# Kernel optimization log

Measured on AMD Instinct MI355X. Metric: run time of the kernel, lower is better.

Reference implementation:

```python
import jax, jax.numpy as jnp
import numpy as np

B, CIN, NF, COUT, H, W = 128, 64, 16, 256, 20, 20


def _warp(features, f):
    # features: (B, Cin, r, c), f: (r, c, 2) flow offsets
    r, c = features.shape[2], features.shape[3]
    grid = jnp.stack(
        jnp.meshgrid(jnp.arange(r, dtype=f.dtype), jnp.arange(c, dtype=f.dtype), indexing='ij'),
        axis=-1,
    )  # (r, c, 2) base index map
    idx = grid + f  # index_map += inverse, inverse == flow[i] after double negation
    base = jnp.floor(idx)
    frac = jax.lax.stop_gradient(idx - base)  # torch detaches s and t
    s, t = frac[..., 0], frac[..., 1]
    b = base.astype(jnp.int32)
    bx, by = b[..., 0], b[..., 1]
    padded = jnp.pad(features, ((0, 0), (0, 0), (1, 1), (1, 1)))  # zero pad by 1

    def gather(ix, iy):
        cx = jnp.clip(ix, 0, r)
        cy = jnp.clip(iy, 0, c)
        return padded[:, :, cx + 1, cy + 1]  # (B, Cin, r, c)

    # NOTE: weight for base_10 is s*(1-t) in the original source (apparent bug,
    # should be (1-s)*t) -- replicated here for faithfulness.
    w00 = (1 - s) * (1 - t)
    w01 = s * (1 - t)
    w10 = s * (1 - t)
    w11 = s * t
    return (gather(bx, by) * w00 + gather(bx + 1, by) * w01
            + gather(bx, by + 1) * w10 + gather(bx + 1, by + 1) * w11)


def setup_inputs() -> dict:
    key = jax.random.key(0)
    k1, k2, k3, k4 = jax.random.split(key, 4)
    x = jax.random.normal(k1, (B, CIN, H, W), dtype=jnp.float32)
    flow = jax.random.normal(k2, (NF, H, W, 2), dtype=jnp.float32)
    combinator = jax.random.normal(k3, (COUT, CIN * NF), dtype=jnp.float32) / np.sqrt(CIN * NF)
    bias = jax.random.normal(k4, (COUT,), dtype=jnp.float32) / np.sqrt(CIN * NF)
    return {"x": x, "flow": flow, "combinator": combinator, "bias": bias}


def reference(x, flow, combinator, bias):
    # per-flow bilinear warp, vectorized over the flow axis
    warped = jax.vmap(lambda f: _warp(x, f))(flow)  # (nf, B, Cin, h, w)
    nf, b, cin, h, w = warped.shape
    # permute(1,3,4,2,0).reshape -> columns ordered channel-major, flow-minor
    feat = warped.transpose(1, 3, 4, 2, 0).reshape(b, h, w, cin * nf)
    out = jnp.einsum('bhwk,ok->bhwo', feat, combinator) + bias
    return out.transpose(0, 3, 1, 2)  # (B, Cout, h, w)
```

## Files before the change

kernel.cpp:

```cpp
#include <hip/hip_runtime.h>
#include <hip/hip_fp16.h>
#include <stdint.h>

#define BATCH 128
#define CIN   64
#define NFLOW 16
#define COUT  256
#define HH    20
#define WW    20
#define NPIX  400
#define KTOT  1024
#define PT    100
#define NPT   4
#define NTH   512
#define NFR   7
#define FLR   112

typedef __attribute__((ext_vector_type(8))) short sh8;
typedef __attribute__((ext_vector_type(4))) float f4;

__global__ void prep_w(const float* __restrict__ wg, __half* __restrict__ Wf) {
    int gid = blockIdx.x * 256 + threadIdx.x;
    int j8  = gid & 127;
    int row = gid >> 7;
    int kc16 = j8 >> 2;
    int h    = j8 & 3;
    __half* dst = Wf + ((size_t)(kc16 * 16 + (row >> 4)) * 64 + h * 16 + (row & 15)) * 8;
    #pragma unroll
    for (int j = 0; j < 8; ++j) {
        int kp = j8 * 8 + j;
        int kc = kp >> 6;
        int l  = kp & 63;
        int f  = (kc >> 3) * 8 + (l >> 3);
        int c  = (kc & 7) * 8 + (l & 7);
        dst[j] = __float2half(wg[(size_t)row * KTOT + c * NFLOW + f]);
    }
}

__global__ __launch_bounds__(NTH, 4) void flow_main(
    const float* __restrict__ xg, const __half* __restrict__ Wf,
    const float* __restrict__ flowg, const float* __restrict__ biasg,
    float* __restrict__ outg)
{
    __shared__ __align__(16) __half xb[CIN * NPIX];
    __shared__ __align__(16) __half fl[2][FLR * 64];

    const int bid0 = blockIdx.x;
    const int bid  = (bid0 & 7) * 64 + (bid0 >> 3);
    const int b  = bid >> 2;
    const int pt = bid & 3;
    const int p0 = pt * PT;

    const int tid  = threadIdx.x;
    const int wv   = tid >> 6;
    const int lane = tid & 63;
    const int lr   = lane & 15;
    const int hq   = lane >> 4;

    const float* xsrc = xg + (size_t)b * (CIN * NPIX);

    #pragma unroll
    for (int it = 0; it < 7; ++it) {
        int idx = it * NTH + tid;
        if (idx < 3200) {
            int cb  = idx / NPIX;
            int pix = idx - cb * NPIX;
            const float* s = xsrc + (size_t)(cb * 8) * NPIX + pix;
            __half2 h0 = __floats2half2_rn(s[0 * NPIX], s[1 * NPIX]);
            __half2 h1 = __floats2half2_rn(s[2 * NPIX], s[3 * NPIX]);
            __half2 h2 = __floats2half2_rn(s[4 * NPIX], s[5 * NPIX]);
            __half2 h3 = __floats2half2_rn(s[6 * NPIX], s[7 * NPIX]);
            uint4 pk;
            pk.x = __builtin_bit_cast(uint32_t, h0);
            pk.y = __builtin_bit_cast(uint32_t, h1);
            pk.z = __builtin_bit_cast(uint32_t, h2);
            pk.w = __builtin_bit_cast(uint32_t, h3);
            *(uint4*)&xb[(size_t)idx * 8] = pk;
        }
    }

    __half2 w2_[2][4];
    int     pb_[2][4];
    int     fo_[2];

    auto build_tables = [&](int fb) {
        #pragma unroll
        for (int it = 0; it < 2; ++it) {
            if (it == 0 || lane < PT - 64) {
                int p  = it * 64 + lane;
                int f  = fb * 8 + wv;
                int gp = p0 + p;
                int i = gp / WW;
                int j = gp - i * WW;
                float fx = flowg[((f * HH + i) * WW + j) * 2 + 0];
                float fy = flowg[((f * HH + i) * WW + j) * 2 + 1];
                float ax = (float)i + fx;
                float ay = (float)j + fy;
                float bxf = floorf(ax), byf = floorf(ay);
                float s = ax - bxf, t = ay - byf;
                int ibx = (int)bxf, iby = (int)byf;
                float w00 = (1.f - s) * (1.f - t);
                float w01 = s * (1.f - t);
                float w10 = s * (1.f - t);
                float w11 = s * t;
                int cx0 = min(max(ibx, 0), HH);
                int cx1 = min(max(ibx + 1, 0), HH);
                int cy0 = min(max(iby, 0), WW);
                int cy1 = min(max(iby + 1, 0), WW);
                int v0 = (cx0 < HH) & (cy0 < WW);
                int v1 = (cx1 < HH) & (cy0 < WW);
                int v2 = (cx0 < HH) & (cy1 < WW);
                int v3 = (cx1 < HH) & (cy1 < WW);
                w2_[it][0] = __half2half2(__float2half(v0 ? w00 : 0.f));
                w2_[it][1] = __half2half2(__float2half(v1 ? w01 : 0.f));
                w2_[it][2] = __half2half2(__float2half(v2 ? w10 : 0.f));
                w2_[it][3] = __half2half2(__float2half(v3 ? w11 : 0.f));
                pb_[it][0] = (v0 ? (cx0 * WW + cy0) : 0) * 16;
                pb_[it][1] = (v1 ? (cx1 * WW + cy0) : 0) * 16;
                pb_[it][2] = (v2 ? (cx0 * WW + cy1) : 0) * 16;
                pb_[it][3] = (v3 ? (cx1 * WW + cy1) : 0) * 16;
                fo_[it] = p * 128 + ((wv ^ (p & 7)) << 4);
            }
        }
    };

    auto fill = [&](int k) {
        const char* xcb = (const char*)xb + (k & 7) * 6400;
        char* flb = (char*)fl[k & 1];
        #pragma unroll
        for (int it = 0; it < 2; ++it) {
            if (it == 0 || lane < PT - 64) {
                __half2 s0 = __builtin_bit_cast(__half2, 0u);
                __half2 s1 = s0, s2 = s0, s3 = s0;
                #pragma unroll
                for (int q = 0; q < 4; ++q) {
                    const uint4 d = *(const uint4*)(xcb + pb_[it][q]);
                    __half2 wq = w2_[it][q];
                    s0 = __hfma2(wq, __builtin_bit_cast(__half2, d.x), s0);
                    s1 = __hfma2(wq, __builtin_bit_cast(__half2, d.y), s1);
                    s2 = __hfma2(wq, __builtin_bit_cast(__half2, d.z), s2);
                    s3 = __hfma2(wq, __builtin_bit_cast(__half2, d.w), s3);
                }
                uint4 pk;
                pk.x = __builtin_bit_cast(uint32_t, s0);
                pk.y = __builtin_bit_cast(uint32_t, s1);
                pk.z = __builtin_bit_cast(uint32_t, s2);
                pk.w = __builtin_bit_cast(uint32_t, s3);
                *(uint4*)(flb + fo_[it]) = pk;
            }
        }
    };

    build_tables(0);
    __syncthreads();
    fill(0);
    __syncthreads();

    f4 acc[2][NFR] = {};

    const int q0 = (hq ^ (lr & 7)) << 4;

    for (int kc = 0; kc < 16; ++kc) {
        if (kc == 7) build_tables(1);

        const sh8* wfp = (const sh8*)Wf + (size_t)(2 * kc * 16 + 2 * wv) * 64 + lane;
        sh8 a00 = wfp[0];
        sh8 a01 = wfp[64];
        sh8 a10 = wfp[1024];
        sh8 a11 = wfp[1088];

        if (kc <= 14) fill(kc + 1);

        const char* flr_b = (const char*)fl[kc & 1];
        __builtin_amdgcn_s_setprio(1);
        #pragma unroll
        for (int nf = 0; nf < NFR; ++nf) {
            int rowb = (nf * 16 + lr) * 128;
            sh8 b0 = *(const sh8*)(flr_b + (rowb + q0));
            acc[0][nf] = __builtin_amdgcn_mfma_f32_16x16x32_f16(a00, b0, acc[0][nf], 0, 0, 0);
            acc[1][nf] = __builtin_amdgcn_mfma_f32_16x16x32_f16(a01, b0, acc[1][nf], 0, 0, 0);
            sh8 b1 = *(const sh8*)(flr_b + ((rowb + q0) ^ 64));
            acc[0][nf] = __builtin_amdgcn_mfma_f32_16x16x32_f16(a10, b1, acc[0][nf], 0, 0, 0);
            acc[1][nf] = __builtin_amdgcn_mfma_f32_16x16x32_f16(a11, b1, acc[1][nf], 0, 0, 0);
        }
        __builtin_amdgcn_s_setprio(0);

        __syncthreads();
    }

    float* ob = outg + (size_t)b * (COUT * NPIX) + p0;
    #pragma unroll
    for (int mi = 0; mi < 2; ++mi) {
        #pragma unroll
        for (int r = 0; r < 4; ++r) {
            int m = (wv * 2 + mi) * 16 + hq * 4 + r;
            float bs = biasg[m];
            #pragma unroll
            for (int nf = 0; nf < NFR; ++nf) {
                if (nf < 6 || lr < 4)
                    ob[(size_t)m * NPIX + nf * 16 + lr] = acc[mi][nf][r] + bs;
            }
        }
    }
}

extern "C" void kernel_launch(void* const* d_in, const int* in_sizes, int n_in,
                              void* d_out, int out_size, void* d_ws, size_t ws_size,
                              hipStream_t stream) {
    const float* x    = (const float*)d_in[0];
    const float* flow = (const float*)d_in[1];
    const float* comb = (const float*)d_in[2];
    const float* bias = (const float*)d_in[3];
    float* out = (float*)d_out;

    __half* Wf = (__half*)d_ws;

    prep_w<<<dim3(128), dim3(256), 0, stream>>>(comb, Wf);
    flow_main<<<dim3(BATCH * NPT), dim3(NTH), 0, stream>>>(x, Wf, flow, bias, out);
}
```

Before: 49.25 us.

## Halve block to 4 waves, each computing 64 output channels

The block shrinks from 8 waves to 4. Each wave now owns 64 output rows (four 16-row M tiles) instead of 32, and builds warp tables for two flows instead of one. Each B fragment loaded from shared memory is reused across four MFMAs instead of two, cutting LDS reads per MFMA and giving more independent MFMA chains. The cost is higher register pressure (twice the accumulators and tables), lower occupancy bound, and twice the per-wave warp-fill and x-staging work.

```diff
diff --git a/kernel.cpp b/kernel.cpp
--- a/kernel.cpp
+++ b/kernel.cpp
@@ -12,7 +12,7 @@
 #define KTOT  1024
 #define PT    100
 #define NPT   4
-#define NTH   512
+#define NTH   256
 #define NFR   7
 #define FLR   112
 
@@ -37,7 +37,7 @@
     }
 }
 
-__global__ __launch_bounds__(NTH, 4) void flow_main(
+__global__ __launch_bounds__(NTH, 2) void flow_main(
     const float* __restrict__ xg, const __half* __restrict__ Wf,
     const float* __restrict__ flowg, const float* __restrict__ biasg,
     float* __restrict__ outg)
@@ -60,7 +60,7 @@
     const float* xsrc = xg + (size_t)b * (CIN * NPIX);
 
     #pragma unroll
-    for (int it = 0; it < 7; ++it) {
+    for (int it = 0; it < 13; ++it) {
         int idx = it * NTH + tid;
         if (idx < 3200) {
             int cb  = idx / NPIX;
@@ -79,16 +79,18 @@
         }
     }
 
-    __half2 w2_[2][4];
-    int     pb_[2][4];
-    int     fo_[2];
+    __half2 w2_[4][4];
+    int     pb_[4][4];
+    int     fo_[4];
 
     auto build_tables = [&](int fb) {
         #pragma unroll
-        for (int it = 0; it < 2; ++it) {
+        for (int g = 0; g < 4; ++g) {
+            int it = g & 1;
             if (it == 0 || lane < PT - 64) {
+                int fi = wv * 2 + (g >> 1);
                 int p  = it * 64 + lane;
-                int f  = fb * 8 + wv;
+                int f  = fb * 8 + fi;
                 int gp = p0 + p;
                 int i = gp / WW;
                 int j = gp - i * WW;
@@ -111,15 +113,15 @@
                 int v1 = (cx1 < HH) & (cy0 < WW);
                 int v2 = (cx0 < HH) & (cy1 < WW);
                 int v3 = (cx1 < HH) & (cy1 < WW);
-                w2_[it][0] = __half2half2(__float2half(v0 ? w00 : 0.f));
-                w2_[it][1] = __half2half2(__float2half(v1 ? w01 : 0.f));
-                w2_[it][2] = __half2half2(__float2half(v2 ? w10 : 0.f));
-                w2_[it][3] = __half2half2(__float2half(v3 ? w11 : 0.f));
-                pb_[it][0] = (v0 ? (cx0 * WW + cy0) : 0) * 16;
-                pb_[it][1] = (v1 ? (cx1 * WW + cy0) : 0) * 16;
-                pb_[it][2] = (v2 ? (cx0 * WW + cy1) : 0) * 16;
-                pb_[it][3] = (v3 ? (cx1 * WW + cy1) : 0) * 16;
-                fo_[it] = p * 128 + ((wv ^ (p & 7)) << 4);
+                w2_[g][0] = __half2half2(__float2half(v0 ? w00 : 0.f));
+                w2_[g][1] = __half2half2(__float2half(v1 ? w01 : 0.f));
+                w2_[g][2] = __half2half2(__float2half(v2 ? w10 : 0.f));
+                w2_[g][3] = __half2half2(__float2half(v3 ? w11 : 0.f));
+                pb_[g][0] = (v0 ? (cx0 * WW + cy0) : 0) * 16;
+                pb_[g][1] = (v1 ? (cx1 * WW + cy0) : 0) * 16;
+                pb_[g][2] = (v2 ? (cx0 * WW + cy1) : 0) * 16;
+                pb_[g][3] = (v3 ? (cx1 * WW + cy1) : 0) * 16;
+                fo_[g] = p * 128 + (((fi) ^ (p & 7)) << 4);
             }
         }
     };
@@ -128,14 +130,15 @@
         const char* xcb = (const char*)xb + (k & 7) * 6400;
         char* flb = (char*)fl[k & 1];
         #pragma unroll
-        for (int it = 0; it < 2; ++it) {
+        for (int g = 0; g < 4; ++g) {
+            int it = g & 1;
             if (it == 0 || lane < PT - 64) {
                 __half2 s0 = __builtin_bit_cast(__half2, 0u);
                 __half2 s1 = s0, s2 = s0, s3 = s0;
                 #pragma unroll
                 for (int q = 0; q < 4; ++q) {
-                    const uint4 d = *(const uint4*)(xcb + pb_[it][q]);
-                    __half2 wq = w2_[it][q];
+                    const uint4 d = *(const uint4*)(xcb + pb_[g][q]);
+                    __half2 wq = w2_[g][q];
                     s0 = __hfma2(wq, __builtin_bit_cast(__half2, d.x), s0);
                     s1 = __hfma2(wq, __builtin_bit_cast(__half2, d.y), s1);
                     s2 = __hfma2(wq, __builtin_bit_cast(__half2, d.z), s2);
@@ -146,7 +149,7 @@
                 pk.y = __builtin_bit_cast(uint32_t, s1);
                 pk.z = __builtin_bit_cast(uint32_t, s2);
                 pk.w = __builtin_bit_cast(uint32_t, s3);
-                *(uint4*)(flb + fo_[it]) = pk;
+                *(uint4*)(flb + fo_[g]) = pk;
             }
         }
     };
@@ -156,18 +159,16 @@
     fill(0);
     __syncthreads();
 
-    f4 acc[2][NFR] = {};
+    f4 acc[4][NFR] = {};
 
     const int q0 = (hq ^ (lr & 7)) << 4;
 
     for (int kc = 0; kc < 16; ++kc) {
         if (kc == 7) build_tables(1);
 
-        const sh8* wfp = (const sh8*)Wf + (size_t)(2 * kc * 16 + 2 * wv) * 64 + lane;
-        sh8 a00 = wfp[0];
-        sh8 a01 = wfp[64];
-        sh8 a10 = wfp[1024];
-        sh8 a11 = wfp[1088];
+        const sh8* wfp = (const sh8*)Wf + (size_t)(2 * kc * 16 + 4 * wv) * 64 + lane;
+        sh8 a0_0 = wfp[0],    a0_1 = wfp[64],   a0_2 = wfp[128],  a0_3 = wfp[192];
+        sh8 a1_0 = wfp[1024], a1_1 = wfp[1088], a1_2 = wfp[1152], a1_3 = wfp[1216];
 
         if (kc <= 14) fill(kc + 1);
 
@@ -177,11 +178,15 @@
         for (int nf = 0; nf < NFR; ++nf) {
             int rowb = (nf * 16 + lr) * 128;
             sh8 b0 = *(const sh8*)(flr_b + (rowb + q0));
-            acc[0][nf] = __builtin_amdgcn_mfma_f32_16x16x32_f16(a00, b0, acc[0][nf], 0, 0, 0);
-            acc[1][nf] = __builtin_amdgcn_mfma_f32_16x16x32_f16(a01, b0, acc[1][nf], 0, 0, 0);
             sh8 b1 = *(const sh8*)(flr_b + ((rowb + q0) ^ 64));
-            acc[0][nf] = __builtin_amdgcn_mfma_f32_16x16x32_f16(a10, b1, acc[0][nf], 0, 0, 0);
-            acc[1][nf] = __builtin_amdgcn_mfma_f32_16x16x32_f16(a11, b1, acc[1][nf], 0, 0, 0);
+            acc[0][nf] = __builtin_amdgcn_mfma_f32_16x16x32_f16(a0_0, b0, acc[0][nf], 0, 0, 0);
+            acc[1][nf] = __builtin_amdgcn_mfma_f32_16x16x32_f16(a0_1, b0, acc[1][nf], 0, 0, 0);
+            acc[2][nf] = __builtin_amdgcn_mfma_f32_16x16x32_f16(a0_2, b0, acc[2][nf], 0, 0, 0);
+            acc[3][nf] = __builtin_amdgcn_mfma_f32_16x16x32_f16(a0_3, b0, acc[3][nf], 0, 0, 0);
+            acc[0][nf] = __builtin_amdgcn_mfma_f32_16x16x32_f16(a1_0, b1, acc[0][nf], 0, 0, 0);
+            acc[1][nf] = __builtin_amdgcn_mfma_f32_16x16x32_f16(a1_1, b1, acc[1][nf], 0, 0, 0);
+            acc[2][nf] = __builtin_amdgcn_mfma_f32_16x16x32_f16(a1_2, b1, acc[2][nf], 0, 0, 0);
+            acc[3][nf] = __builtin_amdgcn_mfma_f32_16x16x32_f16(a1_3, b1, acc[3][nf], 0, 0, 0);
         }
         __builtin_amdgcn_s_setprio(0);
 
@@ -190,10 +195,10 @@
 
     float* ob = outg + (size_t)b * (COUT * NPIX) + p0;
     #pragma unroll
-    for (int mi = 0; mi < 2; ++mi) {
+    for (int mi = 0; mi < 4; ++mi) {
         #pragma unroll
         for (int r = 0; r < 4; ++r) {
-            int m = (wv * 2 + mi) * 16 + hq * 4 + r;
+            int m = wv * 64 + mi * 16 + hq * 4 + r;
             float bs = biasg[m];
             #pragma unroll
             for (int nf = 0; nf < NFR; ++nf) {
```

After: 50.74 us. 3.0% more time.

## Precompute fp16 channel-packed x in a separate kernel and gather from global

Applied to the files above, without the earlier changes.

Adds a prep_x kernel that converts x to fp16 in the channel-packed layout once per batch, replacing the per-block conversion into a 51KB LDS buffer. The main kernel now gathers bilinear taps directly from global/L2 instead of shared memory. This frees LDS, which could raise occupancy, and removes the redundant conversion done by four blocks per batch. The cost is an extra kernel launch plus scattered global loads in the fill stage, which may have higher latency than LDS reads.

```diff
diff --git a/kernel.cpp b/kernel.cpp
--- a/kernel.cpp
+++ b/kernel.cpp
@@ -37,12 +37,30 @@
     }
 }
 
+__global__ void prep_x(const float* __restrict__ xg, __half* __restrict__ xt) {
+    int gid = blockIdx.x * 256 + threadIdx.x;
+    int b   = gid / (8 * NPIX);
+    int r   = gid - b * (8 * NPIX);
+    int cb  = r / NPIX;
+    int pix = r - cb * NPIX;
+    const float* src = xg + (size_t)b * (CIN * NPIX) + (size_t)(cb * 8) * NPIX + pix;
+    __half2 h0 = __floats2half2_rn(src[0 * NPIX], src[1 * NPIX]);
+    __half2 h1 = __floats2half2_rn(src[2 * NPIX], src[3 * NPIX]);
+    __half2 h2 = __floats2half2_rn(src[4 * NPIX], src[5 * NPIX]);
+    __half2 h3 = __floats2half2_rn(src[6 * NPIX], src[7 * NPIX]);
+    uint4 pk;
+    pk.x = __builtin_bit_cast(uint32_t, h0);
+    pk.y = __builtin_bit_cast(uint32_t, h1);
+    pk.z = __builtin_bit_cast(uint32_t, h2);
+    pk.w = __builtin_bit_cast(uint32_t, h3);
+    *(uint4*)&xt[(size_t)gid * 8] = pk;
+}
+
 __global__ __launch_bounds__(NTH, 4) void flow_main(
-    const float* __restrict__ xg, const __half* __restrict__ Wf,
+    const __half* __restrict__ xt, const __half* __restrict__ Wf,
     const float* __restrict__ flowg, const float* __restrict__ biasg,
     float* __restrict__ outg)
 {
-    __shared__ __align__(16) __half xb[CIN * NPIX];
     __shared__ __align__(16) __half fl[2][FLR * 64];
 
     const int bid0 = blockIdx.x;
@@ -57,27 +75,7 @@
     const int lr   = lane & 15;
     const int hq   = lane >> 4;
 
-    const float* xsrc = xg + (size_t)b * (CIN * NPIX);
-
-    #pragma unroll
-    for (int it = 0; it < 7; ++it) {
-        int idx = it * NTH + tid;
-        if (idx < 3200) {
-            int cb  = idx / NPIX;
-            int pix = idx - cb * NPIX;
-            const float* s = xsrc + (size_t)(cb * 8) * NPIX + pix;
-            __half2 h0 = __floats2half2_rn(s[0 * NPIX], s[1 * NPIX]);
-            __half2 h1 = __floats2half2_rn(s[2 * NPIX], s[3 * NPIX]);
-            __half2 h2 = __floats2half2_rn(s[4 * NPIX], s[5 * NPIX]);
-            __half2 h3 = __floats2half2_rn(s[6 * NPIX], s[7 * NPIX]);
-            uint4 pk;
-            pk.x = __builtin_bit_cast(uint32_t, h0);
-            pk.y = __builtin_bit_cast(uint32_t, h1);
-            pk.z = __builtin_bit_cast(uint32_t, h2);
-            pk.w = __builtin_bit_cast(uint32_t, h3);
-            *(uint4*)&xb[(size_t)idx * 8] = pk;
-        }
-    }
+    const char* xtb = (const char*)(xt + (size_t)b * (8 * NPIX * 8));
 
     __half2 w2_[2][4];
     int     pb_[2][4];
@@ -125,7 +123,7 @@
     };
 
     auto fill = [&](int k) {
-        const char* xcb = (const char*)xb + (k & 7) * 6400;
+        const char* xcb = xtb + (k & 7) * 6400;
         char* flb = (char*)fl[k & 1];
         #pragma unroll
         for (int it = 0; it < 2; ++it) {
@@ -152,7 +150,6 @@
     };
 
     build_tables(0);
-    __syncthreads();
     fill(0);
     __syncthreads();
 
@@ -214,7 +211,9 @@
     float* out = (float*)d_out;
 
     __half* Wf = (__half*)d_ws;
+    __half* xt = (__half*)((char*)d_ws + (512 << 10));
 
     prep_w<<<dim3(128), dim3(256), 0, stream>>>(comb, Wf);
-    flow_main<<<dim3(BATCH * NPT), dim3(NTH), 0, stream>>>(x, Wf, flow, bias, out);
-}
+    prep_x<<<dim3(1600), dim3(256), 0, stream>>>(x, xt);
+    flow_main<<<dim3(BATCH * NPT), dim3(NTH), 0, stream>>>(xt, Wf, flow, bias, out);
+}
```

Result: slower. 62.08 us (+26.0%).
